# Performance work log

Hardware: AMD Instinct MI355X
Metric: run time of the kernel (lower is better)

## Reference

```python
import jax, jax.numpy as jnp
import numpy as np

V, E = 50000, 300          # vocab, embedding dim (Word2Vec)
U1, U2, DNS = 256, 256, 128  # lstm1 units, lstm2 units, dense units
B, S = 64, 512             # batch, seq_len


def _glorot(key, shape):
    fan_in, fan_out = shape
    lim = jnp.sqrt(6.0 / (fan_in + fan_out))
    return jax.random.uniform(key, shape, jnp.float32, -lim, lim)


def setup_inputs() -> dict:
    key = jax.random.key(0)
    ks = jax.random.split(key, 12)
    d = {
        'tokens': jax.random.randint(ks[0], (B, S), 0, V),
        'emb': jax.random.normal(ks[1], (V, E), jnp.float32) * 0.05,
        # layer 1 gates: combined dim = E + U1
        'W1f': _glorot(ks[2], (E + U1, U1)), 'b1f': jnp.zeros((U1,), jnp.float32),
        'W1i': _glorot(ks[3], (E + U1, U1)), 'b1i': jnp.zeros((U1,), jnp.float32),
        'W1c': _glorot(ks[4], (E + U1, U1)), 'b1c': jnp.zeros((U1,), jnp.float32),
        'W1o': _glorot(ks[5], (E + U1, U1)), 'b1o': jnp.zeros((U1,), jnp.float32),
        # layer 2 gates: combined dim = U1 + U2
        'W2f': _glorot(ks[6], (U1 + U2, U2)), 'b2f': jnp.zeros((U2,), jnp.float32),
        'W2i': _glorot(ks[7], (U1 + U2, U2)), 'b2i': jnp.zeros((U2,), jnp.float32),
        'W2c': _glorot(ks[8], (U1 + U2, U2)), 'b2c': jnp.zeros((U2,), jnp.float32),
        'W2o': _glorot(ks[9], (U1 + U2, U2)), 'b2o': jnp.zeros((U2,), jnp.float32),
        'Wd': _glorot(ks[10], (U2, DNS)), 'bd': jnp.zeros((DNS,), jnp.float32),
        'Wout': _glorot(ks[11], (DNS, 1)), 'bout': jnp.zeros((1,), jnp.float32),
    }
    return d


def _lstm(x_seq, Wf, bf, Wi, bi, Wc, bc, Wo, bo, units):
    # x_seq: [B, S, D]; scan over time, returns all hidden states [B, S, units]
    b = x_seq.shape[0]
    h0 = jnp.zeros((b, units), x_seq.dtype)
    c0 = jnp.zeros((b, units), x_seq.dtype)

    def step(carry, x_t):
        h, c = carry
        z = jnp.concatenate([x_t, h], axis=-1)           # [B, D+units]
        f = jax.nn.sigmoid(z @ Wf + bf)
        i = jax.nn.sigmoid(z @ Wi + bi)
        g = jnp.tanh(z @ Wc + bc)
        c_new = f * c + i * g
        o = jax.nn.sigmoid(z @ Wo + bo)
        h_new = o * jnp.tanh(c_new)
        return (h_new, c_new), h_new

    (_, _), hs = jax.lax.scan(step, (h0, c0), jnp.swapaxes(x_seq, 0, 1))
    return jnp.swapaxes(hs, 0, 1)  # [B, S, units]


def reference(tokens, emb, W1f, b1f, W1i, b1i, W1c, b1c, W1o, b1o,
              W2f, b2f, W2i, b2i, W2c, b2c, W2o, b2o, Wd, bd, Wout, bout):
    x = emb[tokens]                                       # [B, S, E]
    h1 = _lstm(x, W1f, b1f, W1i, b1i, W1c, b1c, W1o, b1o, U1)   # [B, S, U1]
    h2 = _lstm(h1, W2f, b2f, W2i, b2i, W2c, b2c, W2o, b2o, U2)  # [B, S, U2]
    last = h2[:, -1, :]                                   # return_sequences=False -> final h
    d = jax.nn.relu(last @ Wd + bd)
    return jax.nn.sigmoid(d @ Wout + bout)                # [B, 1]
```

## Files before the change

kernel.cpp:

```cpp
#include <hip/hip_runtime.h>
#include <stdint.h>

typedef __bf16 bf16_t;
typedef __bf16 bf16x8 __attribute__((ext_vector_type(8)));
typedef float floatx16 __attribute__((ext_vector_type(16)));
typedef unsigned int u32;
typedef unsigned long long u64;

#define NPROD 64
#define H1R   8
#define SST   592
#define ZST   1104
#define FP    32

struct KParams {
  const int* tok;
  const float* emb;
  const float* W1[4]; const float* b1[4];
  const float* W2[4]; const float* b2[4];
  const float* Wd; const float* bd; const float* Wout; const float* bout;
  float* out;
  uint16_t* h1;
  uint16_t* h2;
  u32* fl0;
  u32* fl1;
  u32* fl0g;
  u32* pflags;
  float* dstage;
  bf16_t* w1bf;
  float* gx;
  int R;
};

__device__ __forceinline__ float sigf(float x) { return 1.f / (1.f + __expf(-x)); }
__device__ __forceinline__ float tanhf_fast(float x) { return 1.f - 2.f / (__expf(2.f * x) + 1.f); }

__device__ __forceinline__ u32 pack2(float a, float b) {
  uint16_t x = __builtin_bit_cast(uint16_t, (bf16_t)a);
  uint16_t y = __builtin_bit_cast(uint16_t, (bf16_t)b);
  return ((u32)y << 16) | (u32)x;
}
__device__ __forceinline__ float2 u2f2(u64 v) { union { u64 u; float2 f; } x; x.u = v; return x.f; }

__device__ __forceinline__ u32  ald32(const u32* p) { return __hip_atomic_load(p, __ATOMIC_RELAXED, __HIP_MEMORY_SCOPE_AGENT); }
__device__ __forceinline__ void ast32(u32* p, u32 v) { __hip_atomic_store(p, v, __ATOMIC_RELAXED, __HIP_MEMORY_SCOPE_AGENT); }
__device__ __forceinline__ u64  ald64(const u64* p) { return __hip_atomic_load(p, __ATOMIC_RELAXED, __HIP_MEMORY_SCOPE_AGENT); }

template<int NA, int NB>
__device__ __forceinline__ void waitcond(const u32* fa, u32 na, const u32* fb, u32 nb,
                                         const u32* pc, u32 nc) {
  const int lane = threadIdx.x & 63;
  const u32* ap; u32 need;
  if (lane < NA)           { ap = fa + lane * FP;        need = na; }
  else if (lane < NA + NB) { ap = fb + (lane - NA) * FP; need = nb; }
  else                     { ap = pc;                    need = nc; }
  while (!__all(ald32(ap) >= need)) {}
  __atomic_signal_fence(__ATOMIC_ACQUIRE);
}

__device__ __forceinline__ void waitg16(const u32* fa, u32 na) {
  const int lane = threadIdx.x & 63;
  const u32* ap = fa + (lane & 15) * FP;
  while (!__all(ald32(ap) >= na)) {}
  __atomic_signal_fence(__ATOMIC_ACQUIRE);
}

__device__ __forceinline__ void stage_h64(const u64* hp, char* smem) {
  const int tid = threadIdx.x;
  u64 tmp[16];
#pragma unroll
  for (int t = 0; t < 16; ++t) tmp[t] = ald64(hp + tid + 256 * t);
#pragma unroll
  for (int t = 0; t < 16; ++t) {
    int i = tid + 256 * t, b = i >> 6, cc = i & 63;
    *(u64*)(smem + b * SST + cc * 8) = tmp[t];
  }
}

__device__ void run_l0(const KParams& p, int sub, char* abuf, float* cst, float* biasl)
{
  const int tid = threadIdx.x;
  const int w = tid >> 6, l = tid & 63, q = l >> 5, lr = l & 31;
  const int mh = w & 1, nh = w >> 1;

  if (tid < 64) biasl[tid] = p.b1[tid >> 4][sub * 16 + (tid & 15)];

  const int c = nh * 32 + lr;
  const float* Wg = p.W1[c >> 4];
  const int un = sub * 16 + (c & 15);
  bf16x8 wf[16];
#pragma unroll
  for (int s = 0; s < 16; ++s)
#pragma unroll
    for (int j = 0; j < 8; ++j) {
      int k = 16 * s + 8 * q + j;
      wf[s][j] = (bf16_t)Wg[(300 + k) * 256 + un];
    }
  __syncthreads();

  float cs[2][2] = {{0.f, 0.f}, {0.f, 0.f}};

  for (int s = 0; s < 512; ++s) {
    u32 n1 = (s >= 8) ? (u32)(s - 7) : 0u;
    if (w == 0) waitcond<16, 32>(p.fl0, (u32)s, p.fl1, n1, &p.pflags[s * FP], 1u);
    __syncthreads();

    const float* slab = p.gx + (size_t)(s % p.R) * 65536u;
    u64 g[2][4];
#pragma unroll
    for (int kk = 0; kk < 2; ++kk) {
      int pp = tid + 256 * kk, b = pp >> 3, u2 = (pp & 7) * 2;
      const float* gb = slab + b * 1024 + sub * 64 + u2;
      g[kk][0] = ald64((const u64*)gb);
      g[kk][1] = ald64((const u64*)(gb + 16));
      g[kk][2] = ald64((const u64*)(gb + 32));
      g[kk][3] = ald64((const u64*)(gb + 48));
    }
    stage_h64((const u64*)(p.h1 + ((s + H1R - 1) & (H1R - 1)) * 16384), abuf);
    __syncthreads();

    floatx16 acc;
#pragma unroll
    for (int e = 0; e < 16; ++e) acc[e] = 0.f;
    const char* arow = abuf + (mh * 32 + lr) * SST + q * 16;
#pragma unroll
    for (int s2 = 0; s2 < 16; ++s2) {
      bf16x8 af = *(const bf16x8*)(arow + 32 * s2);
      acc = __builtin_amdgcn_mfma_f32_32x32x16_bf16(af, wf[s2], acc, 0, 0, 0);
    }
#pragma unroll
    for (int e = 0; e < 16; ++e) {
      int ri = (e & 3) + 8 * (e >> 2) + 4 * q;
      cst[(mh * 32 + ri) * 68 + nh * 32 + lr] = acc[e];
    }
    __syncthreads();

    uint16_t* hout = p.h1 + (s & (H1R - 1)) * 16384;
#pragma unroll
    for (int kk = 0; kk < 2; ++kk) {
      int pp = tid + 256 * kk, b = pp >> 3, u2 = (pp & 7) * 2;
      float2 pf = *(float2*)&cst[b * 68 +      u2];
      float2 pi = *(float2*)&cst[b * 68 + 16 + u2];
      float2 pg = *(float2*)&cst[b * 68 + 32 + u2];
      float2 po = *(float2*)&cst[b * 68 + 48 + u2];
      float2 gf = u2f2(g[kk][0]), gi = u2f2(g[kk][1]);
      float2 gg = u2f2(g[kk][2]), go = u2f2(g[kk][3]);
      float hv[2];
#pragma unroll
      for (int j = 0; j < 2; ++j) {
        float fj = sigf((j ? pf.y : pf.x) + (j ? gf.y : gf.x) + biasl[u2 + j]);
        float ij = sigf((j ? pi.y : pi.x) + (j ? gi.y : gi.x) + biasl[16 + u2 + j]);
        float gj = tanhf_fast((j ? pg.y : pg.x) + (j ? gg.y : gg.x) + biasl[32 + u2 + j]);
        float oj = sigf((j ? po.y : po.x) + (j ? go.y : go.x) + biasl[48 + u2 + j]);
        float cn = fj * cs[kk][j] + ij * gj;
        cs[kk][j] = cn;
        hv[j] = oj * tanhf_fast(cn);
      }
      ast32((u32*)(hout + b * 256 + sub * 16 + u2), pack2(hv[0], hv[1]));
    }
    __syncthreads();
    if (tid == 0) {
      ast32(&p.fl0[sub * FP], (u32)(s + 1));
      ast32(&p.fl0g[sub * FP], (u32)(s + 1));
    }
  }
}

__device__ void run_l1(const KParams& p, int w2, char* zbuf, float* cst, float* biasl)
{
  const int tid = threadIdx.x;
  const int wv = tid >> 6, l = tid & 63, q = l >> 5, lr = l & 31;
  const int nh = wv & 1, kh = wv >> 1;
  const int bh = w2 & 1, sub1 = w2 >> 1;

  if (tid < 64) biasl[tid] = p.b2[tid >> 4][sub1 * 16 + (tid & 15)];

  const int c = nh * 32 + lr;
  const float* Wg = p.W2[c >> 4];
  const int un = sub1 * 16 + (c & 15);
  bf16x8 wf[16];
#pragma unroll
  for (int s = 0; s < 16; ++s)
#pragma unroll
    for (int j = 0; j < 8; ++j) {
      int k = kh * 256 + s * 16 + q * 8 + j;
      wf[s][j] = (bf16_t)Wg[k * 256 + un];
    }
  __syncthreads();

  float cs2[2] = {0.f, 0.f};
  const int cb = tid >> 3, cu = (tid & 7) * 2;

  for (int s = 0; s < 512; ++s) {
    if (wv == 0) waitcond<32, 16>(p.fl1, (u32)s, p.fl0, (u32)(s + 1), p.fl0, 0u);
    __syncthreads();

    const u64* hp1 = (const u64*)(p.h1 + (s & (H1R - 1)) * 16384) + bh * 2048;
    const u64* hp2 = (const u64*)(p.h2 + ((s + 1) & 1) * 16384) + bh * 2048;
    u64 t1[8], t2[8];
#pragma unroll
    for (int t = 0; t < 8; ++t) t1[t] = ald64(hp1 + tid + 256 * t);
#pragma unroll
    for (int t = 0; t < 8; ++t) t2[t] = ald64(hp2 + tid + 256 * t);
#pragma unroll
    for (int t = 0; t < 8; ++t) {
      int i = tid + 256 * t, r = i >> 6, cc = i & 63;
      *(u64*)(zbuf + r * ZST + cc * 8) = t1[t];
    }
#pragma unroll
    for (int t = 0; t < 8; ++t) {
      int i = tid + 256 * t, r = i >> 6, cc = i & 63;
      *(u64*)(zbuf + r * ZST + 512 + cc * 8) = t2[t];
    }
    __syncthreads();

    floatx16 acc;
#pragma unroll
    for (int e = 0; e < 16; ++e) acc[e] = 0.f;
    const char* arow = zbuf + lr * ZST + kh * 512 + q * 16;
#pragma unroll
    for (int s2 = 0; s2 < 16; ++s2) {
      bf16x8 af = *(const bf16x8*)(arow + 32 * s2);
      acc = __builtin_amdgcn_mfma_f32_32x32x16_bf16(af, wf[s2], acc, 0, 0, 0);
    }
#pragma unroll
    for (int e = 0; e < 16; ++e) {
      int ri = (e & 3) + 8 * (e >> 2) + 4 * q;
      cst[kh * 2176 + ri * 68 + nh * 32 + lr] = acc[e];
    }
    __syncthreads();

    uint16_t* hout = p.h2 + (s & 1) * 16384;
    {
      float2 pf = *(float2*)&cst[cb * 68 +      cu];
      float2 pi = *(float2*)&cst[cb * 68 + 16 + cu];
      float2 pg = *(float2*)&cst[cb * 68 + 32 + cu];
      float2 po = *(float2*)&cst[cb * 68 + 48 + cu];
      float2 qf = *(float2*)&cst[2176 + cb * 68 +      cu];
      float2 qi = *(float2*)&cst[2176 + cb * 68 + 16 + cu];
      float2 qg = *(float2*)&cst[2176 + cb * 68 + 32 + cu];
      float2 qo = *(float2*)&cst[2176 + cb * 68 + 48 + cu];
      float hv[2];
#pragma unroll
      for (int j = 0; j < 2; ++j) {
        float fj = sigf((j ? pf.y + qf.y : pf.x + qf.x) + biasl[cu + j]);
        float ij = sigf((j ? pi.y + qi.y : pi.x + qi.x) + biasl[16 + cu + j]);
        float gj = tanhf_fast((j ? pg.y + qg.y : pg.x + qg.x) + biasl[32 + cu + j]);
        float oj = sigf((j ? po.y + qo.y : po.x + qo.x) + biasl[48 + cu + j]);
        float cn = fj * cs2[j] + ij * gj;
        cs2[j] = cn;
        hv[j] = oj * tanhf_fast(cn);
      }
      ast32((u32*)(hout + (bh * 32 + cb) * 256 + sub1 * 16 + cu), pack2(hv[0], hv[1]));
    }
    __syncthreads();
    if (tid == 0) ast32(&p.fl1[w2 * FP], (u32)(s + 1));
  }

  if (wv == 0) waitcond<32, 0>(p.fl1, 512u, p.fl1, 0u, p.fl1, 0u);
  __syncthreads();
  {
    const u64* hp = (const u64*)(p.h2 + 16384);
    u64 tmp[16];
#pragma unroll
    for (int t = 0; t < 16; ++t) tmp[t] = ald64(hp + tid + 256 * t);
#pragma unroll
    for (int t = 0; t < 16; ++t) {
      int i = tid + 256 * t, b = i >> 6, cc = i & 63;
      *(u64*)(zbuf + b * 520 + cc * 8) = tmp[t];
    }
  }
  __syncthreads();
  {
    int b = tid >> 2, cc = w2 * 4 + (tid & 3);
    const bf16_t* hrow = (const bf16_t*)(zbuf + b * 520);
    float a = p.bd[cc];
#pragma unroll 8
    for (int k = 0; k < 256; ++k) a += (float)hrow[k] * p.Wd[k * 128 + cc];
    ast32((u32*)&p.dstage[b * 128 + cc], __builtin_bit_cast(u32, fmaxf(a, 0.f)));
  }
  __syncthreads();
  if (tid == 0) ast32(&p.fl1[w2 * FP], 513u);

  if (w2 == 0) {
    if (wv == 0) waitcond<32, 0>(p.fl1, 513u, p.fl1, 0u, p.fl1, 0u);
    __syncthreads();
    if (tid < 64) {
      float a = p.bout[0];
#pragma unroll 8
      for (int cc = 0; cc < 128; ++cc) {
        u32 dv = ald32((u32*)&p.dstage[tid * 128 + cc]);
        a += __builtin_bit_cast(float, dv) * p.Wout[cc];
      }
      p.out[tid] = sigf(a);
    }
  }
}

__device__ void run_prod(const KParams& p, int pw, char* smem)
{
  const int tid = threadIdx.x;
  const int w = tid >> 6, l = tid & 63, q = l >> 5, lr = l & 31;
  const int mh = w & 1, chalf = w >> 1;
  const int R = p.R;

  for (int jj = 0; jj < 512 / NPROD; ++jj) {
    const int s = pw + NPROD * jj;
    if (s >= R) {
      if (w == 0) waitg16(p.fl0g, (u32)(s - R + 1));
    }
    __syncthreads();
    {
      int b = tid >> 2, qq = tid & 3;
      int tokv = p.tok[b * 512 + s];
      const float4* src = (const float4*)(p.emb + (size_t)tokv * 300);
      char* dst = smem + b * 656;
      for (int j2 = qq; j2 < 75; j2 += 4) {
        float4 v = src[j2];
        *(u32*)(dst + 8 * j2)     = pack2(v.x, v.y);
        *(u32*)(dst + 8 * j2 + 4) = pack2(v.z, v.w);
      }
      for (int i = tid; i < 640; i += 256) {
        int bb = i / 10, cc2 = i % 10;
        *(u32*)(smem + bb * 656 + 600 + cc2 * 4) = 0u;
      }
    }
    __syncthreads();

    bf16x8 afr[20];
    const char* arow = smem + (mh * 32 + lr) * 656 + q * 16;
#pragma unroll
    for (int kt = 0; kt < 20; ++kt) afr[kt] = *(const bf16x8*)(arow + 32 * kt);

    float* slab = p.gx + (size_t)(s % R) * 65536u;
    for (int c2 = 0; c2 < 16; ++c2) {
      int n = (chalf * 16 + c2) * 32 + lr;
      floatx16 acc;
#pragma unroll
      for (int e = 0; e < 16; ++e) acc[e] = 0.f;
#pragma unroll
      for (int kt = 0; kt < 20; ++kt) {
        bf16x8 bf = ((const bf16x8*)p.w1bf)[(kt * 1024 + n) * 2 + q];
        acc = __builtin_amdgcn_mfma_f32_32x32x16_bf16(afr[kt], bf, acc, 0, 0, 0);
      }
#pragma unroll
      for (int e = 0; e < 16; ++e) {
        int ri = (e & 3) + 8 * (e >> 2) + 4 * q;
        ast32((u32*)(slab + (mh * 32 + ri) * 1024 + n), __builtin_bit_cast(u32, acc[e]));
      }
    }
    __syncthreads();
    if (tid == 0) ast32(&p.pflags[s * FP], 1u);
  }
}

__global__ __launch_bounds__(256, 1) void lstm_main(KParams p)
{
  __shared__ __align__(16) char smem[64 * 656];
  __shared__ float cst[4352];
  __shared__ float biasl[64];
  const int wg = blockIdx.x;
  if (wg < 16)       run_l0(p, wg, smem, cst, biasl);
  else if (wg < 48)  run_l1(p, wg - 16, smem, cst, biasl);
  else               run_prod(p, wg - 48, smem);
}

__global__ void prep_w(KParams p) {
  int idx = blockIdx.x * 256 + threadIdx.x;
  if (idx >= 20 * 1024 * 16) return;
  int kk = idx & 15, n = (idx >> 4) & 1023, kt = idx >> 14;
  int k = kt * 16 + kk;
  int g = (n >> 4) & 3, su = n >> 6, u = n & 15;
  float v = (k < 300) ? p.W1[g][k * 256 + su * 16 + u] : 0.f;
  p.w1bf[idx] = (bf16_t)v;
}

__global__ void init_ws(u32* ws32) {
  int i = blockIdx.x * 256 + threadIdx.x;
  if (i < 100352) ws32[i] = 0u;
}

extern "C" void kernel_launch(void* const* d_in, const int* in_sizes, int n_in,
                              void* d_out, int out_size, void* d_ws, size_t ws_size,
                              hipStream_t stream)
{
  KParams p;
  p.tok = (const int*)d_in[0];
  p.emb = (const float*)d_in[1];
  for (int g = 0; g < 4; ++g) {
    p.W1[g] = (const float*)d_in[2 + 2 * g];
    p.b1[g] = (const float*)d_in[3 + 2 * g];
    p.W2[g] = (const float*)d_in[10 + 2 * g];
    p.b2[g] = (const float*)d_in[11 + 2 * g];
  }
  p.Wd   = (const float*)d_in[18];
  p.bd   = (const float*)d_in[19];
  p.Wout = (const float*)d_in[20];
  p.bout = (const float*)d_in[21];
  p.out  = (float*)d_out;

  char* ws = (char*)d_ws;
  p.h1     = (uint16_t*)ws;
  p.h2     = (uint16_t*)(ws + 262144);
  p.fl0    = (u32*)(ws + 327680);
  p.fl1    = (u32*)(ws + 329728);
  p.fl0g   = (u32*)(ws + 333824);
  p.pflags = (u32*)(ws + 335872);
  p.dstage = (float*)(ws + 401408);
  p.w1bf   = (bf16_t*)(ws + 434176);
  p.gx     = (float*)(ws + 1089536);

  long avail = (long)ws_size - 1089536L;
  int R = (int)(avail / 262144L);
  if (R > 64) R = 64;
  if (R < 1)  R = 1;
  p.R = R;

  hipLaunchKernelGGL(init_ws, dim3(392), dim3(256), 0, stream, (u32*)d_ws);
  hipLaunchKernelGGL(prep_w, dim3(1280), dim3(256), 0, stream, p);
  hipLaunchKernelGGL(lstm_main, dim3(16 + 32 + NPROD), dim3(256), 0, stream, p);
}
```

Baseline: 1.860 ms.

## Prefetch next-step layer-1 h1 tile and narrow layer-2 flag waits

Layer-2 blocks now wait on the layer-1 producer flags and load the next timestep's h1 slice into registers right after publishing their own output, taking that load off the critical path of the next step. The per-step wait in wave 0 now polls only the 16 layer-2 flags sharing the same batch half instead of all 32 plus the layer-1 flags. The polling loop is restructured to keep two loads in flight. This adds per-thread register pressure and makes every wave spin on flags after each step, which could contend with the memory system.

After: 1.876 ms. Within noise of the previous version (+0.8%).

```diff
diff --git a/kernel.cpp b/kernel.cpp
--- a/kernel.cpp
+++ b/kernel.cpp
@@ -46,6 +46,11 @@
 __device__ __forceinline__ void ast32(u32* p, u32 v) { __hip_atomic_store(p, v, __ATOMIC_RELAXED, __HIP_MEMORY_SCOPE_AGENT); }
 __device__ __forceinline__ u64  ald64(const u64* p) { return __hip_atomic_load(p, __ATOMIC_RELAXED, __HIP_MEMORY_SCOPE_AGENT); }
 
+#define PIPE_POLL(ap, need)                                            \
+  { u32 _f0 = ald32(ap), _f1 = ald32(ap);                              \
+    for (;;) { if (__all(_f0 >= (need))) break; _f0 = _f1; _f1 = ald32(ap); } \
+    __atomic_signal_fence(__ATOMIC_ACQUIRE); }
+
 template<int NA, int NB>
 __device__ __forceinline__ void waitcond(const u32* fa, u32 na, const u32* fb, u32 nb,
                                          const u32* pc, u32 nc) {
@@ -54,27 +59,13 @@
   if (lane < NA)           { ap = fa + lane * FP;        need = na; }
   else if (lane < NA + NB) { ap = fb + (lane - NA) * FP; need = nb; }
   else                     { ap = pc;                    need = nc; }
-  while (!__all(ald32(ap) >= need)) {}
-  __atomic_signal_fence(__ATOMIC_ACQUIRE);
+  PIPE_POLL(ap, need)
 }
 
 __device__ __forceinline__ void waitg16(const u32* fa, u32 na) {
   const int lane = threadIdx.x & 63;
   const u32* ap = fa + (lane & 15) * FP;
-  while (!__all(ald32(ap) >= na)) {}
-  __atomic_signal_fence(__ATOMIC_ACQUIRE);
-}
-
-__device__ __forceinline__ void stage_h64(const u64* hp, char* smem) {
-  const int tid = threadIdx.x;
-  u64 tmp[16];
-#pragma unroll
-  for (int t = 0; t < 16; ++t) tmp[t] = ald64(hp + tid + 256 * t);
-#pragma unroll
-  for (int t = 0; t < 16; ++t) {
-    int i = tid + 256 * t, b = i >> 6, cc = i & 63;
-    *(u64*)(smem + b * SST + cc * 8) = tmp[t];
-  }
+  PIPE_POLL(ap, na)
 }
 
 __device__ void run_l0(const KParams& p, int sub, char* abuf, float* cst, float* biasl)
@@ -90,11 +81,11 @@
   const int un = sub * 16 + (c & 15);
   bf16x8 wf[16];
 #pragma unroll
-  for (int s = 0; s < 16; ++s)
+  for (int s2 = 0; s2 < 16; ++s2)
 #pragma unroll
     for (int j = 0; j < 8; ++j) {
-      int k = 16 * s + 8 * q + j;
-      wf[s][j] = (bf16_t)Wg[(300 + k) * 256 + un];
+      int k = 16 * s2 + 8 * q + j;
+      wf[s2][j] = (bf16_t)Wg[(300 + k) * 256 + un];
     }
   __syncthreads();
 
@@ -116,7 +107,17 @@
       g[kk][2] = ald64((const u64*)(gb + 32));
       g[kk][3] = ald64((const u64*)(gb + 48));
     }
-    stage_h64((const u64*)(p.h1 + ((s + H1R - 1) & (H1R - 1)) * 16384), abuf);
+    {
+      const u64* hp = (const u64*)(p.h1 + ((s + H1R - 1) & (H1R - 1)) * 16384);
+      u64 tmp[16];
+#pragma unroll
+      for (int t = 0; t < 16; ++t) tmp[t] = ald64(hp + tid + 256 * t);
+#pragma unroll
+      for (int t = 0; t < 16; ++t) {
+        int i = tid + 256 * t, b = i >> 6, cc = i & 63;
+        *(u64*)(abuf + b * SST + cc * 8) = tmp[t];
+      }
+    }
     __syncthreads();
 
     floatx16 acc;
@@ -180,26 +181,37 @@
   const int un = sub1 * 16 + (c & 15);
   bf16x8 wf[16];
 #pragma unroll
-  for (int s = 0; s < 16; ++s)
+  for (int s2 = 0; s2 < 16; ++s2)
 #pragma unroll
     for (int j = 0; j < 8; ++j) {
-      int k = kh * 256 + s * 16 + q * 8 + j;
-      wf[s][j] = (bf16_t)Wg[k * 256 + un];
+      int k = kh * 256 + s2 * 16 + q * 8 + j;
+      wf[s2][j] = (bf16_t)Wg[k * 256 + un];
     }
   __syncthreads();
 
   float cs2[2] = {0.f, 0.f};
   const int cb = tid >> 3, cu = (tid & 7) * 2;
 
+  {
+    const u32* ap = p.fl0 + (l & 15) * FP;
+    PIPE_POLL(ap, 1u)
+  }
+  u64 t1[8];
+  {
+    const u64* hp1 = (const u64*)p.h1 + bh * 2048;
+#pragma unroll
+    for (int t = 0; t < 8; ++t) t1[t] = ald64(hp1 + tid + 256 * t);
+  }
+
   for (int s = 0; s < 512; ++s) {
-    if (wv == 0) waitcond<32, 16>(p.fl1, (u32)s, p.fl0, (u32)(s + 1), p.fl0, 0u);
-    __syncthreads();
-
-    const u64* hp1 = (const u64*)(p.h1 + (s & (H1R - 1)) * 16384) + bh * 2048;
+    if (wv == 0) {
+      const u32* ap = p.fl1 + (2 * (l & 15) + bh) * FP;
+      PIPE_POLL(ap, (u32)s)
+    }
+    __syncthreads();
+
     const u64* hp2 = (const u64*)(p.h2 + ((s + 1) & 1) * 16384) + bh * 2048;
-    u64 t1[8], t2[8];
-#pragma unroll
-    for (int t = 0; t < 8; ++t) t1[t] = ald64(hp1 + tid + 256 * t);
+    u64 t2[8];
 #pragma unroll
     for (int t = 0; t < 8; ++t) t2[t] = ald64(hp2 + tid + 256 * t);
 #pragma unroll
@@ -230,7 +242,6 @@
     }
     __syncthreads();
 
-    uint16_t* hout = p.h2 + (s & 1) * 16384;
     {
       float2 pf = *(float2*)&cst[cb * 68 +      cu];
       float2 pi = *(float2*)&cst[cb * 68 + 16 + cu];
@@ -251,10 +262,19 @@
         cs2[j] = cn;
         hv[j] = oj * tanhf_fast(cn);
       }
+      uint16_t* hout = p.h2 + (s & 1) * 16384;
       ast32((u32*)(hout + (bh * 32 + cb) * 256 + sub1 * 16 + cu), pack2(hv[0], hv[1]));
     }
     __syncthreads();
     if (tid == 0) ast32(&p.fl1[w2 * FP], (u32)(s + 1));
+
+    if (s < 511) {
+      const u32* ap = p.fl0 + (l & 15) * FP;
+      PIPE_POLL(ap, (u32)(s + 2))
+      const u64* hpn = (const u64*)(p.h1 + ((s + 1) & (H1R - 1)) * 16384) + bh * 2048;
+#pragma unroll
+      for (int t = 0; t < 8; ++t) t1[t] = ald64(hpn + tid + 256 * t);
+    }
   }
 
   if (wv == 0) waitcond<32, 0>(p.fl1, 512u, p.fl1, 0u, p.fl1, 0u);
```
